# Optimization experiments

Hardware: AMD Instinct MI355X
Metric: run time of the kernel (lower is better)

The kernel has to match this reference:

```python
import jax, jax.numpy as jnp
import numpy as np

N_USERS = 100000
N_ITEMS = 100000
D = 64
B = 2048


def _ancf_layer(q, keys, aW, ab, W1, W2):
    # AttentionMechanism: hidden = relu(keys @ aW.T + ab)  [N, d]
    hidden = jax.nn.relu(keys @ aW.T + ab)
    # scores [B, N]; softmax over keys (dim=1)
    attn = jax.nn.softmax(q @ hidden.T, axis=1)
    q2 = q + attn @ keys  # [B, d]
    # MessageAggregation loop collapsed algebraically:
    # out = W1(q2) + sum_j W1(k_j) + sum_j W2(q2 * k_j)
    #     = W1(q2) + W1(S) + W2(q2 * S),  S = sum_j k_j
    S = keys.sum(axis=0)  # [d]
    out = (q2 + S) @ W1.T + (q2 * S) @ W2.T
    return jax.nn.leaky_relu(out, 0.01)


def setup_inputs() -> dict:
    key = jax.random.key(0)
    ks = jax.random.split(key, 12)
    scale_emb = 0.1
    scale_w = (2.0 / (D + D)) ** 0.5  # xavier-normal std for square layers
    inp = {
        "user_emb": jax.random.normal(ks[0], (N_USERS, D), jnp.float32) * scale_emb,
        "item_emb": jax.random.normal(ks[1], (N_ITEMS, D), jnp.float32) * scale_emb,
        "u_attn_W": jax.random.normal(ks[2], (D, D), jnp.float32) * scale_w,
        "u_attn_b": jnp.zeros((D,), jnp.float32),
        "u_W1": jax.random.normal(ks[3], (D, D), jnp.float32) * scale_w,
        "u_W2": jax.random.normal(ks[4], (D, D), jnp.float32) * scale_w,
        "i_attn_W": jax.random.normal(ks[5], (D, D), jnp.float32) * scale_w,
        "i_attn_b": jnp.zeros((D,), jnp.float32),
        "i_W1": jax.random.normal(ks[6], (D, D), jnp.float32) * scale_w,
        "i_W2": jax.random.normal(ks[7], (D, D), jnp.float32) * scale_w,
        "user_id": jax.random.randint(ks[8], (B,), 0, N_USERS),
        "item_id": jax.random.randint(ks[9], (B,), 0, N_ITEMS),
        "all_user_ids": jnp.arange(N_USERS),
        "all_item_ids": jnp.arange(N_ITEMS),
    }
    return inp


def reference(user_emb, item_emb, u_attn_W, u_attn_b, u_W1, u_W2,
              i_attn_W, i_attn_b, i_W1, i_W2,
              user_id, item_id, all_user_ids, all_item_ids):
    all_user_embeddings = user_emb[all_user_ids]  # [N_users, d]
    all_item_embeddings = item_emb[all_item_ids]  # [N_items, d]
    ue = all_user_embeddings[user_id]  # [B, d]
    ie = all_item_embeddings[item_id]  # [B, d]

    ue_out = _ancf_layer(ue, all_item_embeddings, u_attn_W, u_attn_b, u_W1, u_W2)
    ie_out = _ancf_layer(ie, all_user_embeddings, i_attn_W, i_attn_b, i_W1, i_W2)

    og_user = jnp.concatenate([ue, ue_out], axis=1)  # [B, 2d]
    og_item = jnp.concatenate([ie, ie_out], axis=1)  # [B, 2d]
    return og_user.T @ og_item  # [2d, 2d]
```

## Files before the change

### kernel.cpp

```cpp
#include <hip/hip_runtime.h>


typedef __bf16 bf16x8 __attribute__((ext_vector_type(8)));
typedef float f32x2 __attribute__((ext_vector_type(2)));
typedef float f32x4 __attribute__((ext_vector_type(4)));
typedef float f32x16 __attribute__((ext_vector_type(16)));
typedef unsigned int u32x4 __attribute__((ext_vector_type(4)));
typedef int i32x4 __attribute__((ext_vector_type(4)));
typedef int i32x8 __attribute__((ext_vector_type(8)));

static constexpr int NKEYS  = 100000;
static constexpr int NP     = 102400;
static constexpr int DIM    = 64;
static constexpr int BQ     = 2048;
static constexpr int NCH    = 32;
static constexpr int CHROWS = NP / NCH;
static constexpr int NPH    = CHROWS / 64;
static constexpr int NTIL   = NP / 64;
static constexpr float PADCNT = float(NP - NKEYS);
static constexpr float LOG2E  = 1.44269504088896340736f;

#define DEVINL __device__ __forceinline__

DEVINL unsigned int cvtpk(float lo, float hi) {
    unsigned int r;
    asm("v_cvt_pk_bf16_f32 %0, %1, %2" : "=v"(r) : "v"(lo), "v"(hi));
    return r;
}
DEVINL unsigned short bfr(float f) {
    return (unsigned short)(cvtpk(f, f) & 0xffffu);
}
DEVINL float bf2f(unsigned short u) {
    unsigned int w = (unsigned int)u << 16;
    return __builtin_bit_cast(float, w);
}
DEVINL void permswap(unsigned int& a, unsigned int& b) {
    asm("v_permlane32_swap_b32 %0, %1" : "+v"(a), "+v"(b));
}
DEVINL bf16x8 pack_frag(unsigned int w0, unsigned int w1, unsigned int w2, unsigned int w3) {
    u32x4 t; t[0] = w0; t[1] = w1; t[2] = w2; t[3] = w3;
    return __builtin_bit_cast(bf16x8, t);
}
DEVINL bf16x8 frag8_f32(const float* p) {
    f32x4 a = *reinterpret_cast<const f32x4*>(p);
    f32x4 b = *reinterpret_cast<const f32x4*>(p + 4);
    return pack_frag(cvtpk(a[0], a[1]), cvtpk(a[2], a[3]),
                     cvtpk(b[0], b[1]), cvtpk(b[2], b[3]));
}
DEVINL unsigned int fp8x4(float a, float b, float c, float d) {
    int r = __builtin_amdgcn_cvt_pk_fp8_f32(a, b, 0, false);
    r = __builtin_amdgcn_cvt_pk_fp8_f32(c, d, r, true);
    return (unsigned int)r;
}
DEVINL unsigned char fp8b(float f) {
    return (unsigned char)(__builtin_amdgcn_cvt_pk_fp8_f32(f, f, 0, false) & 0xFF);
}
DEVINL i32x8 ld8(const unsigned char* lo, const unsigned char* hi) {
    union { i32x8 v; i32x4 h[2]; } u;
    u.h[0] = *reinterpret_cast<const i32x4*>(lo);
    u.h[1] = *reinterpret_cast<const i32x4*>(hi);
    return u.v;
}
DEVINL f32x16 mfma8(i32x8 a, i32x8 b, f32x16 c) {
    return __builtin_amdgcn_mfma_scale_f32_32x32x64_f8f6f4(
        a, b, c, 0 , 0 ,
        0, 0x7F7F7F7F, 0, 0x7F7F7F7F);
}
DEVINL float fexp2(float x) {
    float f = __builtin_fmaf(x, 8388608.0f, 1065713994.0f);
    int i = (int)f;
    return __builtin_bit_cast(float, i);
}
DEVINL f32x2 pkadd(f32x2 a, f32x2 b) {
    f32x2 r;
    asm("v_pk_add_f32 %0, %1, %2" : "=v"(r) : "v"(a), "v"(b));
    return r;
}

__global__ __launch_bounds__(256) void prep_kernel(
    const float* __restrict__ user_emb, const float* __restrict__ item_emb,
    const float* __restrict__ uaW, const float* __restrict__ uab,
    const float* __restrict__ iaW, const float* __restrict__ iab,
    unsigned char* __restrict__ Khid, unsigned char* __restrict__ Vpan,
    float* __restrict__ csum)
{
    const int side = blockIdx.y;
    const int tile = blockIdx.x;
    const float* keys = (side == 0) ? item_emb : user_emb;
    const float* aW   = (side == 0) ? uaW : iaW;
    const float* ab   = (side == 0) ? uab : iab;
    unsigned char* Kh  = Khid + (size_t)side * NP * DIM;
    unsigned char* Vps = Vpan + (size_t)side * (NP / 32) * 2048;

    __shared__ float Kf[64][68];
    __shared__ float Wf[64][68];
    __shared__ float bl[64];

    const int t  = threadIdx.x;
    const int r  = t >> 2;
    const int c0 = (t & 3) * 16;

    {
        const float4* src = reinterpret_cast<const float4*>(aW + r * 64 + c0);
        float4* dst = reinterpret_cast<float4*>(&Wf[r][c0]);
        #pragma unroll
        for (int q = 0; q < 4; ++q) dst[q] = src[q];
        if (t < 64) bl[t] = ab[t];
    }
    {
        const int n = tile * 64 + r;
        float4* dst = reinterpret_cast<float4*>(&Kf[r][c0]);
        if (n < NKEYS) {
            const float4* src = reinterpret_cast<const float4*>(keys + (size_t)n * 64 + c0);
            #pragma unroll
            for (int q = 0; q < 4; ++q) dst[q] = src[q];
        } else {
            const float4 z = make_float4(0.f, 0.f, 0.f, 0.f);
            #pragma unroll
            for (int q = 0; q < 4; ++q) dst[q] = z;
        }
    }
    __syncthreads();

    {
        const int wv = t >> 6, lane = t & 63;
        const int c = lane & 31, hi = lane >> 5;
        const int n0 = (wv & 1) * 32, j0 = (wv >> 1) * 32;
        f32x16 acc{};
        #pragma unroll
        for (int ks = 0; ks < 4; ++ks) {
            bf16x8 af = frag8_f32(&Kf[n0 + c][ks * 16 + hi * 8]);
            bf16x8 bf_ = frag8_f32(&Wf[j0 + c][ks * 16 + hi * 8]);
            acc = __builtin_amdgcn_mfma_f32_32x32x16_bf16(af, bf_, acc, 0, 0, 0);
        }
        const float bj = bl[j0 + c];
        #pragma unroll
        for (int rr = 0; rr < 16; ++rr) {
            const int n  = n0 + (rr & 3) + 8 * (rr >> 2) + 4 * hi;
            const int gn = tile * 64 + n;
            float h = fmaxf(acc[rr] + bj, 0.f);
            if (gn >= NKEYS) h = 0.f;
            Kh[(size_t)gn * 64 + j0 + c] = fp8b(h);
        }
    }
    {
        unsigned int pw[4];
        #pragma unroll
        for (int j = 0; j < 4; ++j)
            pw[j] = fp8x4(Kf[c0 + 4 * j][r],     Kf[c0 + 4 * j + 1][r],
                          Kf[c0 + 4 * j + 2][r], Kf[c0 + 4 * j + 3][r]);
        unsigned char* dst = Vps + ((size_t)(2 * tile + (c0 >> 5))) * 2048 + r * 32 + (c0 & 31);
        *reinterpret_cast<uint4*>(dst) = make_uint4(pw[0], pw[1], pw[2], pw[3]);
    }
    if (t < 64) {
        float s = 0.f;
        #pragma unroll 8
        for (int rr = 0; rr < 64; ++rr) s += Kf[rr][t];
        csum[((size_t)side * NTIL + tile) * 64 + t] = s;
    }
}

__global__ __launch_bounds__(64) void sreduceA_kernel(const float* __restrict__ csum,
                                                      float* __restrict__ csum2)
{
    const int j = blockIdx.x, side = blockIdx.y, d = threadIdx.x;
    float s = 0.f;
    for (int idx = j; idx < NTIL; idx += 64)
        s += csum[((size_t)side * NTIL + idx) * 64 + d];
    csum2[((size_t)side * 64 + j) * 64 + d] = s;
}

__global__ __launch_bounds__(64) void sreduceB_kernel(const float* __restrict__ csum2,
                                                      float* __restrict__ Sbuf)
{
    const int side = blockIdx.x, d = threadIdx.x;
    float s = 0.f;
    #pragma unroll 8
    for (int j = 0; j < 64; ++j) s += csum2[((size_t)side * 64 + j) * 64 + d];
    Sbuf[side * 64 + d] = s;
}

__global__ __launch_bounds__(256) void wtrans_kernel(
    const float* __restrict__ uW1, const float* __restrict__ uW2,
    const float* __restrict__ iW1, const float* __restrict__ iW2,
    float* __restrict__ WT)
{
    const float* W = (blockIdx.x == 0) ? uW1 : (blockIdx.x == 1) ? uW2
                   : (blockIdx.x == 2) ? iW1 : iW2;
    float* T = WT + (size_t)blockIdx.x * 4096;
    const int t = threadIdx.x;
    const int j = t >> 2;
    const int dd0 = (t & 3) * 16;
    #pragma unroll
    for (int k = 0; k < 16; ++k)
        T[(dd0 + k) * 64 + j] = W[j * 64 + dd0 + k];
}

__global__ __launch_bounds__(512) void flash_kernel(
    const float* __restrict__ user_emb, const float* __restrict__ item_emb,
    const int* __restrict__ user_id, const int* __restrict__ item_id,
    const unsigned char* __restrict__ Khid, const unsigned char* __restrict__ Vpan,
    unsigned short* __restrict__ Opart, float* __restrict__ lpart)
{
    const int side  = blockIdx.z;
    const int chunk = blockIdx.x;
    const int qblk  = blockIdx.y;
    const int wave  = threadIdx.x >> 6;
    const int lane  = threadIdx.x & 63;
    const int c  = lane & 31;
    const int hi = lane >> 5;

    __shared__ __align__(16) unsigned char KV[3][8192];

    const float* emb = (side == 0) ? user_emb : item_emb;
    const int* ids   = (side == 0) ? user_id  : item_id;
    const unsigned char* Kh = Khid + ((size_t)side * NP + (size_t)chunk * CHROWS) * 64;
    const unsigned char* Vb = Vpan + ((size_t)side * (NP / 32) + (size_t)chunk * (CHROWS / 32)) * 2048;

    const unsigned char* gsrc;
    if (wave < 4) {
        const int st = wave >> 1, qh = wave & 1;
        gsrc = Kh + st * 2048 + qh * 16 + c * 64 + hi * 32;
    } else {
        const int dblk = (wave - 4) >> 1, qh = wave & 1;
        gsrc = Vb + dblk * 1024 + qh * 16 + hi * 2048 + c * 32;
    }

    const unsigned char* gnext = gsrc;
    int ibuf = 0;
    auto ISSUE = [&]() {
        __builtin_amdgcn_global_load_lds(
            (const __attribute__((address_space(1))) unsigned int*)gnext,
            (__attribute__((address_space(3))) unsigned int*)&KV[ibuf][wave * 1024],
            16, 0, 0);
        gnext += 4096;
        ibuf = (ibuf == 2) ? 0 : ibuf + 1;
    };

    ISSUE();
    ISSUE();

    const int qtile = qblk * 256 + wave * 32;
    const int id = ids[qtile + c];
    const float* qrow = emb + (size_t)id * 64 + hi * 32;
    i32x8 bq;
    #pragma unroll
    for (int w = 0; w < 8; ++w) {
        float4 f = *reinterpret_cast<const float4*>(qrow + w * 4);
        bq[w] = (int)fp8x4(f.x * LOG2E, f.y * LOG2E, f.z * LOG2E, f.w * LOG2E);
    }

    f32x16 o0{}, o1{};
    f32x2 lacc0{}, lacc1{};

    asm volatile("s_waitcnt vmcnt(1)" ::: "memory");
    __builtin_amdgcn_s_barrier();

    int cbuf = 0;
    for (int p = 0; p < NPH; ++p) {
        if (p + 2 < NPH) ISSUE();

        const unsigned char* Bp = &KV[cbuf][0];
        cbuf = (cbuf == 2) ? 0 : cbuf + 1;
        const int fo = hi * 512 + c * 16;

        i32x8 ak0 = ld8(Bp + fo,        Bp + 1024 + fo);
        i32x8 ak1 = ld8(Bp + 2048 + fo, Bp + 3072 + fo);

        __builtin_amdgcn_s_setprio(1);
        f32x16 z{};
        f32x16 s0 = mfma8(ak0, bq, z);
        f32x16 s1 = mfma8(ak1, bq, z);
        __builtin_amdgcn_s_setprio(0);

        i32x8 bv0 = ld8(Bp + 4096 + fo, Bp + 5120 + fo);
        i32x8 bv1 = ld8(Bp + 6144 + fo, Bp + 7168 + fo);

        #pragma unroll
        for (int rr = 0; rr < 16; ++rr) s0[rr] = fexp2(s0[rr]);
        #pragma unroll
        for (int rr = 0; rr < 16; ++rr) s1[rr] = fexp2(s1[rr]);

        #pragma unroll
        for (int g = 0; g < 8; ++g) {
            f32x2 a; a[0] = s0[2 * g]; a[1] = s0[2 * g + 1];
            f32x2 b; b[0] = s1[2 * g]; b[1] = s1[2 * g + 1];
            if (g & 1) lacc1 = pkadd(lacc1, pkadd(a, b));
            else       lacc0 = pkadd(lacc0, pkadd(a, b));
        }

        union { i32x8 v; unsigned int w[8]; } pu;
        #pragma unroll
        for (int g = 0; g < 4; ++g) {
            pu.w[2 * g]     = fp8x4(s0[4 * g], s0[4 * g + 1], s0[4 * g + 2], s0[4 * g + 3]);
            pu.w[2 * g + 1] = fp8x4(s1[4 * g], s1[4 * g + 1], s1[4 * g + 2], s1[4 * g + 3]);
            permswap(pu.w[2 * g], pu.w[2 * g + 1]);
        }

        __builtin_amdgcn_s_setprio(1);
        o0 = mfma8(pu.v, bv0, o0);
        o1 = mfma8(pu.v, bv1, o1);
        __builtin_amdgcn_s_setprio(0);

        if (p + 1 < NPH) {
            if (p + 2 < NPH) asm volatile("s_waitcnt vmcnt(1)" ::: "memory");
            else             asm volatile("s_waitcnt vmcnt(0)" ::: "memory");
            __builtin_amdgcn_s_barrier();
        }
    }

    float ls = (lacc0[0] + lacc0[1]) + (lacc1[0] + lacc1[1]);
    ls += __shfl_xor(ls, 32);

    unsigned short* Op = Opart + (((size_t)(side * BQ + qtile)) * NCH + chunk) * 64;
    #pragma unroll
    for (int rr = 0; rr < 16; ++rr) {
        const int q = (rr & 3) + 8 * (rr >> 2) + 4 * hi;
        Op[(size_t)q * NCH * 64 + c]      = bfr(o0[rr]);
        Op[(size_t)q * NCH * 64 + 32 + c] = bfr(o1[rr]);
    }
    if (hi == 0)
        lpart[((size_t)(side * BQ + qtile + c)) * NCH + chunk] = ls;
}

__global__ __launch_bounds__(256) void combine_kernel(
    const float* __restrict__ user_emb, const float* __restrict__ item_emb,
    const int* __restrict__ user_id, const int* __restrict__ item_id,
    const float* __restrict__ WT,
    const unsigned short* __restrict__ Opart, const float* __restrict__ lpart,
    const float* __restrict__ Sbuf,
    float* __restrict__ Aog, float* __restrict__ Bog)
{
    const int bid  = blockIdx.x;
    const int side = bid >> 9;
    const int wave = threadIdx.x >> 6;
    const int lane = threadIdx.x & 63;
    const int q    = ((bid & 511) << 2) + wave;
    const int j    = lane;

    const unsigned short* Ob = Opart + ((size_t)(side * BQ + q)) * (NCH * 64) + j;
    float num = 0.f;
    #pragma unroll 8
    for (int ch = 0; ch < NCH; ++ch)
        num += bf2f(Ob[ch * 64]);

    float lv = (lane < NCH) ? lpart[((size_t)(side * BQ + q)) * NCH + lane] : 0.f;
    #pragma unroll
    for (int m = 32; m >= 1; m >>= 1) lv += __shfl_xor(lv, m);
    const float lsum = lv - PADCNT * fexp2(0.0f);

    const int id = ((side == 0) ? user_id : item_id)[q];
    const float* emb = (side == 0) ? user_emb : item_emb;
    const float e  = emb[(size_t)id * 64 + j];
    const float q2 = e + num / lsum;
    const float Sd = Sbuf[side * 64 + j];

    __shared__ float a1s[4][64], a2s[4][64];
    a1s[wave][j] = q2 + Sd;
    a2s[wave][j] = q2 * Sd;

    const float* W1T = WT + (size_t)side * 8192;
    const float* W2T = W1T + 4096;
    float acc = 0.f;
    #pragma unroll 8
    for (int dd = 0; dd < 64; ++dd)
        acc += a1s[wave][dd] * W1T[dd * 64 + j] + a2s[wave][dd] * W2T[dd * 64 + j];
    const float out = (acc >= 0.f) ? acc : 0.01f * acc;

    float* og = (side == 0) ? Aog : Bog;
    og[(size_t)q * 128 + j]      = e;
    og[(size_t)q * 128 + 64 + j] = out;
}

__global__ __launch_bounds__(256) void final1_kernel(
    const float* __restrict__ Aog, const float* __restrict__ Bog, float* __restrict__ part)
{
    const int b = blockIdx.x;
    const int t = threadIdx.x;
    __shared__ float As[16][128];
    __shared__ float Bs[16][128];
    {
        float* Asf = &As[0][0];
        float* Bsf = &Bs[0][0];
        const float* Ab = Aog + (size_t)b * 16 * 128;
        const float* Bb = Bog + (size_t)b * 16 * 128;
        #pragma unroll
        for (int qq = 0; qq < 2; ++qq) {
            const int off = qq * 1024 + t * 4;
            *reinterpret_cast<float4*>(Asf + off) = *reinterpret_cast<const float4*>(Ab + off);
            *reinterpret_cast<float4*>(Bsf + off) = *reinterpret_cast<const float4*>(Bb + off);
        }
    }
    __syncthreads();

    const int i0 = (t >> 4) * 8, j0 = (t & 15) * 8;
    float acc[8][8] = {};
    #pragma unroll
    for (int k = 0; k < 16; ++k) {
        float av[8], bv[8];
        *reinterpret_cast<f32x4*>(&av[0]) = *reinterpret_cast<const f32x4*>(&As[k][i0]);
        *reinterpret_cast<f32x4*>(&av[4]) = *reinterpret_cast<const f32x4*>(&As[k][i0 + 4]);
        *reinterpret_cast<f32x4*>(&bv[0]) = *reinterpret_cast<const f32x4*>(&Bs[k][j0]);
        *reinterpret_cast<f32x4*>(&bv[4]) = *reinterpret_cast<const f32x4*>(&Bs[k][j0 + 4]);
        #pragma unroll
        for (int ii = 0; ii < 8; ++ii)
            #pragma unroll
            for (int jj = 0; jj < 8; ++jj)
                acc[ii][jj] += av[ii] * bv[jj];
    }
    float* P = part + (size_t)b * 128 * 128;
    #pragma unroll
    for (int ii = 0; ii < 8; ++ii) {
        *reinterpret_cast<float4*>(P + (i0 + ii) * 128 + j0)     = *reinterpret_cast<float4*>(&acc[ii][0]);
        *reinterpret_cast<float4*>(P + (i0 + ii) * 128 + j0 + 4) = *reinterpret_cast<float4*>(&acc[ii][4]);
    }
}

__global__ __launch_bounds__(128) void final2_kernel(const float* __restrict__ part,
                                                     float* __restrict__ out)
{
    const int i = blockIdx.x, j = threadIdx.x;
    float s = 0.f;
    #pragma unroll 8
    for (int b = 0; b < 128; ++b) s += part[(size_t)b * 128 * 128 + i * 128 + j];
    out[i * 128 + j] = s;
}

extern "C" void kernel_launch(void* const* d_in, const int* in_sizes, int n_in,
                              void* d_out, int out_size, void* d_ws, size_t ws_size,
                              hipStream_t stream)
{
    (void)in_sizes; (void)n_in; (void)out_size; (void)ws_size;
    const float* user_emb = (const float*)d_in[0];
    const float* item_emb = (const float*)d_in[1];
    const float* uaW = (const float*)d_in[2];
    const float* uab = (const float*)d_in[3];
    const float* uW1 = (const float*)d_in[4];
    const float* uW2 = (const float*)d_in[5];
    const float* iaW = (const float*)d_in[6];
    const float* iab = (const float*)d_in[7];
    const float* iW1 = (const float*)d_in[8];
    const float* iW2 = (const float*)d_in[9];
    const int* user_id = (const int*)d_in[10];
    const int* item_id = (const int*)d_in[11];

    char* ws = (char*)d_ws;
    size_t off = 0;
    auto alloc = [&](size_t bytes) -> void* {
        void* p = ws + off;
        off = (off + bytes + 255) & ~(size_t)255;
        return p;
    };
    unsigned char* Khid8 = (unsigned char*)alloc((size_t)2 * NP * DIM);
    unsigned char* Vpan8 = (unsigned char*)alloc((size_t)2 * (NP / 32) * 2048);
    float* csum  = (float*)alloc((size_t)2 * NTIL * 64 * 4);
    float* csum2 = (float*)alloc((size_t)2 * 64 * 64 * 4);
    float* Sbuf  = (float*)alloc((size_t)2 * 64 * 4);
    float* WT    = (float*)alloc((size_t)4 * 4096 * 4);
    unsigned short* Opart = (unsigned short*)alloc((size_t)2 * BQ * NCH * 64 * 2);
    float* lpart = (float*)alloc((size_t)2 * BQ * NCH * 4);
    float* Aog   = (float*)alloc((size_t)BQ * 128 * 4);
    float* Bog   = (float*)alloc((size_t)BQ * 128 * 4);
    float* Fpart = (float*)alloc((size_t)128 * 128 * 128 * 4);

    prep_kernel<<<dim3(NTIL, 2), 256, 0, stream>>>(user_emb, item_emb, uaW, uab, iaW, iab,
                                                   Khid8, Vpan8, csum);
    sreduceA_kernel<<<dim3(64, 2), 64, 0, stream>>>(csum, csum2);
    sreduceB_kernel<<<2, 64, 0, stream>>>(csum2, Sbuf);
    wtrans_kernel<<<4, 256, 0, stream>>>(uW1, uW2, iW1, iW2, WT);
    flash_kernel<<<dim3(NCH, BQ / 256, 2), 512, 0, stream>>>(user_emb, item_emb, user_id, item_id,
                                                             Khid8, Vpan8, Opart, lpart);
    combine_kernel<<<2 * BQ / 4, 256, 0, stream>>>(user_emb, item_emb, user_id, item_id,
                                                   WT, Opart, lpart, Sbuf, Aog, Bog);
    final1_kernel<<<128, 256, 0, stream>>>(Aog, Bog, Fpart);
    final2_kernel<<<128, 128, 0, stream>>>(Fpart, (float*)d_out);
}
```

Measured before the change: 127.3 us.

## Software-pipeline flash loop so QK of one phase overlaps PV of the previous

Restructures the attention chunk loop so that each phase issues the QK MFMAs for tile p together with the PV MFMAs for tile p-1, which use the fp8-packed probabilities computed in the previous phase. This lets the exp2, row-sum and fp8 packing of one tile overlap with matrix work on another, instead of serialising QK, softmax and PV within each tile. The LDS ring grows from three to four 8 KB buffers so the V panel of the previous tile stays resident while new tiles stream in. The cost is more LDS per block, more live registers from the two packed-probability sets, and a hand-written prologue and epilogue that are tied to the phase count.

```diff
diff --git a/kernel.cpp b/kernel.cpp
--- a/kernel.cpp
+++ b/kernel.cpp
@@ -210,7 +210,7 @@
     const int c  = lane & 31;
     const int hi = lane >> 5;
 
-    __shared__ __align__(16) unsigned char KV[3][8192];
+    __shared__ __align__(16) unsigned char KV[4][8192];
 
     const float* emb = (side == 0) ? user_emb : item_emb;
     const int* ids   = (side == 0) ? user_id  : item_id;
@@ -234,7 +234,7 @@
             (__attribute__((address_space(3))) unsigned int*)&KV[ibuf][wave * 1024],
             16, 0, 0);
         gnext += 4096;
-        ibuf = (ibuf == 2) ? 0 : ibuf + 1;
+        ibuf = (ibuf + 1) & 3;
     };
 
     ISSUE();
@@ -252,61 +252,91 @@
 
     f32x16 o0{}, o1{};
     f32x2 lacc0{}, lacc1{};
+    const int fo = hi * 512 + c * 16;
+
+    auto SMPACK = [&](f32x16 s0, f32x16 s1, i32x8& pa) {
+        #pragma unroll
+        for (int rr = 0; rr < 16; ++rr) s0[rr] = fexp2(s0[rr]);
+        #pragma unroll
+        for (int rr = 0; rr < 16; ++rr) s1[rr] = fexp2(s1[rr]);
+        #pragma unroll
+        for (int g = 0; g < 8; ++g) {
+            f32x2 a; a[0] = s0[2 * g]; a[1] = s0[2 * g + 1];
+            f32x2 b; b[0] = s1[2 * g]; b[1] = s1[2 * g + 1];
+            if (g & 1) lacc1 = pkadd(lacc1, pkadd(a, b));
+            else       lacc0 = pkadd(lacc0, pkadd(a, b));
+        }
+        union { i32x8 v; unsigned int w[8]; } pu;
+        #pragma unroll
+        for (int g = 0; g < 4; ++g) {
+            pu.w[2 * g]     = fp8x4(s0[4 * g], s0[4 * g + 1], s0[4 * g + 2], s0[4 * g + 3]);
+            pu.w[2 * g + 1] = fp8x4(s1[4 * g], s1[4 * g + 1], s1[4 * g + 2], s1[4 * g + 3]);
+            permswap(pu.w[2 * g], pu.w[2 * g + 1]);
+        }
+        pa = pu.v;
+    };
+
+    auto PHASE = [&](int p, const i32x8& paUse, i32x8& paOut, bool do_barrier) {
+        const unsigned char* Bp = &KV[p & 3][0];
+        const unsigned char* Bv = &KV[(p - 1) & 3][0];
+        if (p + 2 < NPH) ISSUE();
+
+        i32x8 ak0 = ld8(Bp + fo,        Bp + 1024 + fo);
+        i32x8 ak1 = ld8(Bp + 2048 + fo, Bp + 3072 + fo);
+        i32x8 bv0 = ld8(Bv + 4096 + fo, Bv + 5120 + fo);
+        i32x8 bv1 = ld8(Bv + 6144 + fo, Bv + 7168 + fo);
+
+        __builtin_amdgcn_s_setprio(1);
+        f32x16 z{};
+        f32x16 s0 = mfma8(ak0, bq, z);
+        f32x16 s1 = mfma8(ak1, bq, z);
+        o0 = mfma8(paUse, bv0, o0);
+        o1 = mfma8(paUse, bv1, o1);
+        __builtin_amdgcn_s_setprio(0);
+
+        SMPACK(s0, s1, paOut);
+
+        if (do_barrier) {
+            if (p + 2 < NPH) asm volatile("s_waitcnt vmcnt(1)" ::: "memory");
+            else             asm volatile("s_waitcnt vmcnt(0)" ::: "memory");
+            __builtin_amdgcn_s_barrier();
+        }
+    };
 
     asm volatile("s_waitcnt vmcnt(1)" ::: "memory");
     __builtin_amdgcn_s_barrier();
 
-    int cbuf = 0;
-    for (int p = 0; p < NPH; ++p) {
-        if (p + 2 < NPH) ISSUE();
-
-        const unsigned char* Bp = &KV[cbuf][0];
-        cbuf = (cbuf == 2) ? 0 : cbuf + 1;
-        const int fo = hi * 512 + c * 16;
-
+    i32x8 paA{}, paB{};
+
+    {
+        const unsigned char* Bp = &KV[0][0];
+        ISSUE();
         i32x8 ak0 = ld8(Bp + fo,        Bp + 1024 + fo);
         i32x8 ak1 = ld8(Bp + 2048 + fo, Bp + 3072 + fo);
-
         __builtin_amdgcn_s_setprio(1);
         f32x16 z{};
         f32x16 s0 = mfma8(ak0, bq, z);
         f32x16 s1 = mfma8(ak1, bq, z);
         __builtin_amdgcn_s_setprio(0);
-
-        i32x8 bv0 = ld8(Bp + 4096 + fo, Bp + 5120 + fo);
-        i32x8 bv1 = ld8(Bp + 6144 + fo, Bp + 7168 + fo);
-
-        #pragma unroll
-        for (int rr = 0; rr < 16; ++rr) s0[rr] = fexp2(s0[rr]);
-        #pragma unroll
-        for (int rr = 0; rr < 16; ++rr) s1[rr] = fexp2(s1[rr]);
-
-        #pragma unroll
-        for (int g = 0; g < 8; ++g) {
-            f32x2 a; a[0] = s0[2 * g]; a[1] = s0[2 * g + 1];
-            f32x2 b; b[0] = s1[2 * g]; b[1] = s1[2 * g + 1];
-            if (g & 1) lacc1 = pkadd(lacc1, pkadd(a, b));
-            else       lacc0 = pkadd(lacc0, pkadd(a, b));
-        }
-
-        union { i32x8 v; unsigned int w[8]; } pu;
-        #pragma unroll
-        for (int g = 0; g < 4; ++g) {
-            pu.w[2 * g]     = fp8x4(s0[4 * g], s0[4 * g + 1], s0[4 * g + 2], s0[4 * g + 3]);
-            pu.w[2 * g + 1] = fp8x4(s1[4 * g], s1[4 * g + 1], s1[4 * g + 2], s1[4 * g + 3]);
-            permswap(pu.w[2 * g], pu.w[2 * g + 1]);
-        }
-
-        __builtin_amdgcn_s_setprio(1);
-        o0 = mfma8(pu.v, bv0, o0);
-        o1 = mfma8(pu.v, bv1, o1);
-        __builtin_amdgcn_s_setprio(0);
-
-        if (p + 1 < NPH) {
-            if (p + 2 < NPH) asm volatile("s_waitcnt vmcnt(1)" ::: "memory");
-            else             asm volatile("s_waitcnt vmcnt(0)" ::: "memory");
-            __builtin_amdgcn_s_barrier();
-        }
+        SMPACK(s0, s1, paA);
+        asm volatile("s_waitcnt vmcnt(1)" ::: "memory");
+        __builtin_amdgcn_s_barrier();
+    }
+
+    for (int pp = 0; pp < (NPH - 2) / 2; ++pp) {
+        const int p = 1 + 2 * pp;
+        PHASE(p,     paA, paB, true);
+        PHASE(p + 1, paB, paA, true);
+    }
+
+    PHASE(NPH - 1, paA, paB, false);
+
+    {
+        const unsigned char* Bv = &KV[(NPH - 1) & 3][0];
+        i32x8 bv0 = ld8(Bv + 4096 + fo, Bv + 5120 + fo);
+        i32x8 bv1 = ld8(Bv + 6144 + fo, Bv + 7168 + fo);
+        o0 = mfma8(paB, bv0, o0);
+        o1 = mfma8(paB, bv1, o1);
     }
 
     float ls = (lacc0[0] + lacc0[1]) + (lacc1[0] + lacc1[1]);
```

After: 141.6 us. +11.2%, slower.
